# Performance work log

Hardware: AMD Instinct MI355X
Metric: run time of the kernel (lower is better)

Reference implementation:

```python
import jax, jax.numpy as jnp
import numpy as np

H = 1024  # lstm_hidden_dim
E = 1024  # embedding_size
T = 512   # seq_len
B = 128   # batch


def setup_inputs() -> dict:
    key = jax.random.key(0)
    k0, k1, k2, k3 = jax.random.split(key, 4)
    bound = 1.0 / np.sqrt(H)
    embeds = jax.random.normal(k0, (T, B, E), dtype=jnp.float32)
    # Stacked gate weights in order [g, i, f, o]; same math as 8 separate GEMMs.
    W_x = jax.random.uniform(k1, (E, 4 * H), jnp.float32, -bound, bound)
    W_h = jax.random.uniform(k2, (H, 4 * H), jnp.float32, -bound, bound)
    b = jax.random.uniform(k3, (4 * H,), jnp.float32, -bound, bound)
    b = b.at[2 * H:3 * H].add(1.0)  # forget-gate bias +1
    return {"embeds": embeds, "W_x": W_x, "W_h": W_h, "b": b}


def reference(embeds, W_x, W_h, b):
    Tn, Bn, _ = embeds.shape
    # Batch all input projections into one big GEMM (same math as per-step GEMMs).
    xproj = jnp.einsum('tbe,ef->tbf', embeds, W_x) + b  # [T, B, 4H]
    h0 = jnp.zeros((Bn, H), embeds.dtype)
    c0 = jnp.zeros((Bn, H), embeds.dtype)

    def step(carry, xp):
        h, c = carry
        z = xp + h @ W_h  # [B, 4H]
        g = jnp.tanh(z[:, :H])
        i = jax.nn.sigmoid(z[:, H:2 * H])
        f = jax.nn.sigmoid(z[:, 2 * H:3 * H])
        o = jax.nn.sigmoid(z[:, 3 * H:])
        c_new = g * i + c * f
        h_new = jnp.tanh(c_new) * o
        # Original module records h BEFORE the update at step t (h_prev).
        return (h_new, c_new), h

    _, h_total = jax.lax.scan(step, (h0, c0), xproj)
    return h_total  # [T, B, H], h_total[0] is zeros
```

## Files before the change

### kernel.cpp

```cpp
#include <hip/hip_runtime.h>
#include <hip/hip_bf16.h>

typedef __attribute__((ext_vector_type(8)))  short          bf16x8;
typedef __attribute__((ext_vector_type(4)))  float          f32x4;
typedef __attribute__((ext_vector_type(8)))  unsigned short us8;

__device__ __forceinline__ unsigned short f2b(float f) {
  union { __hip_bfloat16 h; unsigned short u; } v;
  v.h = __float2bfloat16(f);
  return v.u;
}
__device__ __forceinline__ float b2f(unsigned short u) {
  union { unsigned u; float f; } v; v.u = ((unsigned)u) << 16; return v.f;
}
__device__ __forceinline__ float sigf(float x) {
  return __builtin_amdgcn_rcpf(1.f + __expf(-x));
}
__device__ __forceinline__ float tanhf_(float x) {
  return 2.f * __builtin_amdgcn_rcpf(1.f + __expf(-2.f * x)) - 1.f;
}


__global__ __launch_bounds__(256) void conv_e(const float* __restrict__ in,
                                              unsigned short* __restrict__ out) {
  const size_t i = ((size_t)blockIdx.x * 256 + threadIdx.x) * 8;
  const float4 v0 = *(const float4*)(in + i);
  const float4 v1 = *(const float4*)(in + i + 4);
  us8 o;
  o[0]=f2b(v0.x); o[1]=f2b(v0.y); o[2]=f2b(v0.z); o[3]=f2b(v0.w);
  o[4]=f2b(v1.x); o[5]=f2b(v1.y); o[6]=f2b(v1.z); o[7]=f2b(v1.w);
  *(us8*)(out + i) = o;
}

__global__ __launch_bounds__(256) void conv_wT(const float* __restrict__ W,
                                               unsigned short* __restrict__ WT) {
  __shared__ float tile[64][65];
  const int bx = blockIdx.x & 63;
  const int by = blockIdx.x >> 6;
  const int tc = threadIdx.x & 63, tr = threadIdx.x >> 6;
  #pragma unroll
  for (int i = 0; i < 16; ++i) {
    const int r = i * 4 + tr;
    tile[r][tc] = W[(size_t)(by * 64 + r) * 4096 + bx * 64 + tc];
  }
  __syncthreads();
  #pragma unroll
  for (int i = 0; i < 16; ++i) {
    const int c = i * 4 + tr;
    WT[(size_t)(bx * 64 + c) * 1024 + by * 64 + tc] = f2b(tile[tc][c]);
  }
}

__global__ __launch_bounds__(256) void conv_whp(const float* __restrict__ Wh,
                                                unsigned short* __restrict__ Wp) {
  const int id = blockIdx.x * 256 + threadIdx.x;
  const int l  = id & 63;
  const int kt = (id >> 6) & 7;
  const int nt = (id >> 9) & 7;
  const int kq = (id >> 12) & 3;
  const int n  = id >> 14;
  const int zi = nt * 16 + (l & 15);
  const int col = (zi >> 5) * 1024 + n * 32 + (zi & 31);
  const int k0 = kq * 256 + kt * 32 + (l >> 4) * 8;
  us8 o;
  #pragma unroll
  for (int j = 0; j < 8; ++j) o[j] = f2b(Wh[(size_t)(k0 + j) * 4096 + col]);
  *(us8*)(Wp + (size_t)id * 8) = o;
}

__global__ __launch_bounds__(256) void gemm_xproj(const unsigned short* __restrict__ A,
                                                  const unsigned short* __restrict__ B,
                                                  unsigned short* __restrict__ C) {
  __shared__ unsigned short Alds[128 * 64];
  __shared__ unsigned short Blds[128 * 64];
  const int tid = threadIdx.x, lane = tid & 63, wv = tid >> 6;
  const int wm = wv >> 1, wn = wv & 1;
  const int bn = blockIdx.x & 31, bm = blockIdx.x >> 5;
  f32x4 acc[4][4] = {};
  const int srow = wv * 8 + (lane >> 3);
  const int sinner = (lane & 7) * 8;
  for (int kt = 0; kt < 16; ++kt) {
    #pragma unroll
    for (int rd = 0; rd < 4; ++rd) {
      const int row = rd * 32 + srow;
      const unsigned short* ga = A + (size_t)(bm * 128 + row) * 1024 + kt * 64 + sinner;
      const unsigned short* gb = B + (size_t)(bn * 128 + row) * 1024 + kt * 64 + sinner;
      __builtin_amdgcn_global_load_lds(
          (const __attribute__((address_space(1))) unsigned short*)ga,
          (__attribute__((address_space(3))) unsigned short*)(Alds + rd * 2048 + wv * 512),
          16, 0, 0);
      __builtin_amdgcn_global_load_lds(
          (const __attribute__((address_space(1))) unsigned short*)gb,
          (__attribute__((address_space(3))) unsigned short*)(Blds + rd * 2048 + wv * 512),
          16, 0, 0);
    }
    __syncthreads();
    #pragma unroll
    for (int ks = 0; ks < 2; ++ks) {
      const int kk = ks * 32 + (lane >> 4) * 8;
      bf16x8 af[4], bfr[4];
      #pragma unroll
      for (int mt = 0; mt < 4; ++mt)
        af[mt] = *(const bf16x8*)(Alds + (wm * 64 + mt * 16 + (lane & 15)) * 64 + kk);
      #pragma unroll
      for (int nt = 0; nt < 4; ++nt)
        bfr[nt] = *(const bf16x8*)(Blds + (wn * 64 + nt * 16 + (lane & 15)) * 64 + kk);
      #pragma unroll
      for (int mt = 0; mt < 4; ++mt)
        #pragma unroll
        for (int nt = 0; nt < 4; ++nt)
          acc[mt][nt] = __builtin_amdgcn_mfma_f32_16x16x32_bf16(af[mt], bfr[nt], acc[mt][nt], 0, 0, 0);
    }
    __syncthreads();
  }
  #pragma unroll
  for (int mt = 0; mt < 4; ++mt) {
    const int row0 = bm * 128 + wm * 64 + mt * 16 + (lane >> 4) * 4;
    #pragma unroll
    for (int nt = 0; nt < 4; ++nt) {
      const int col = bn * 128 + wn * 64 + nt * 16 + (lane & 15);
      #pragma unroll
      for (int r = 0; r < 4; ++r)
        C[(size_t)(row0 + r) * 4096 + col] = f2b(acc[mt][nt][r]);
    }
  }
}

__global__ __launch_bounds__(256, 1) void lstm_recur(
    const unsigned short* __restrict__ xproj,
    const unsigned short* __restrict__ Wp,
    const float* __restrict__ bias,
    unsigned short* __restrict__ hbuf,
    float* __restrict__ out,
    unsigned* __restrict__ flags) {
  __shared__ float zpart[10][16][132];
  const int tid = threadIdx.x;
  const int lane = tid & 63;
  const int kq = tid >> 6;
  const int m = blockIdx.x >> 5;
  const int n = blockIdx.x & 31;

  bf16x8 wf[64];
  {
    const unsigned short* wb = Wp + ((size_t)(n * 4 + kq) * 64) * 512 + lane * 8;
    #pragma unroll
    for (int f = 0; f < 64; ++f) wf[f] = *(const bf16x8*)(wb + f * 512);
  }

  const int r    = tid >> 4;
  const int hg   = tid & 15;
  const int hc0  = n * 32 + hg * 2;
  const int grow = m * 16 + r;

  const float2 bb0 = *(const float2*)(bias +        hc0);
  const float2 bb1 = *(const float2*)(bias + 1024 + hc0);
  const float2 bb2 = *(const float2*)(bias + 2048 + hc0);
  const float2 bb3 = *(const float2*)(bias + 3072 + hc0);

  float cr0 = 0.f, cr1 = 0.f;
  const size_t xbase = (size_t)grow * 4096 + hc0;
  unsigned* bcast = flags + (m * 32 + (lane & 31)) * 32 + n;
  const unsigned* myf = flags + (size_t)(m * 32 + n) * 32 + (lane & 31);

  unsigned xu0, xu1, xu2, xu3;
  {
    const unsigned short* xpp = xproj + xbase;
    asm volatile("global_load_dword %0, %1, off" : "=v"(xu0) : "v"(xpp));
    asm volatile("global_load_dword %0, %1, off" : "=v"(xu1) : "v"(xpp + 1024));
    asm volatile("global_load_dword %0, %1, off" : "=v"(xu2) : "v"(xpp + 2048));
    asm volatile("global_load_dword %0, %1, off" : "=v"(xu3) : "v"(xpp + 3072));
  }

  const size_t aoff = ((size_t)(m * 16 + (lane & 15))) * 1024 + kq * 256 + (lane >> 4) * 8;

  for (int t = 0; t < 511; ++t) {
    const unsigned short* ab = hbuf + (t & 1) * 131072 + aoff;

    bf16x8 av0, av1, av2, av3, av4, av5, av6, av7;
    __builtin_amdgcn_sched_barrier(0);
    asm volatile("global_load_dwordx4 %0, %1, off sc0 sc1"            : "=v"(av0) : "v"(ab));
    asm volatile("global_load_dwordx4 %0, %1, off offset:64 sc0 sc1"  : "=v"(av1) : "v"(ab));
    asm volatile("global_load_dwordx4 %0, %1, off offset:128 sc0 sc1" : "=v"(av2) : "v"(ab));
    asm volatile("global_load_dwordx4 %0, %1, off offset:192 sc0 sc1" : "=v"(av3) : "v"(ab));
    asm volatile("global_load_dwordx4 %0, %1, off offset:256 sc0 sc1" : "=v"(av4) : "v"(ab));
    asm volatile("global_load_dwordx4 %0, %1, off offset:320 sc0 sc1" : "=v"(av5) : "v"(ab));
    asm volatile("global_load_dwordx4 %0, %1, off offset:384 sc0 sc1" : "=v"(av6) : "v"(ab));
    asm volatile("global_load_dwordx4 %0, %1, off offset:448 sc0 sc1" : "=v"(av7) : "v"(ab));
    asm volatile("s_waitcnt vmcnt(0)" ::: "memory");
    __builtin_amdgcn_sched_barrier(0);

    f32x4 ac0 = {0.f,0.f,0.f,0.f}, ac1 = {0.f,0.f,0.f,0.f};
    f32x4 ac2 = {0.f,0.f,0.f,0.f}, ac3 = {0.f,0.f,0.f,0.f};
    f32x4 ac4 = {0.f,0.f,0.f,0.f}, ac5 = {0.f,0.f,0.f,0.f};
    f32x4 ac6 = {0.f,0.f,0.f,0.f}, ac7 = {0.f,0.f,0.f,0.f};
#define MF_STEP(AV, KT) \
    ac0 = __builtin_amdgcn_mfma_f32_16x16x32_bf16(AV, wf[ 0 + KT], ac0, 0, 0, 0); \
    ac1 = __builtin_amdgcn_mfma_f32_16x16x32_bf16(AV, wf[ 8 + KT], ac1, 0, 0, 0); \
    ac2 = __builtin_amdgcn_mfma_f32_16x16x32_bf16(AV, wf[16 + KT], ac2, 0, 0, 0); \
    ac3 = __builtin_amdgcn_mfma_f32_16x16x32_bf16(AV, wf[24 + KT], ac3, 0, 0, 0); \
    ac4 = __builtin_amdgcn_mfma_f32_16x16x32_bf16(AV, wf[32 + KT], ac4, 0, 0, 0); \
    ac5 = __builtin_amdgcn_mfma_f32_16x16x32_bf16(AV, wf[40 + KT], ac5, 0, 0, 0); \
    ac6 = __builtin_amdgcn_mfma_f32_16x16x32_bf16(AV, wf[48 + KT], ac6, 0, 0, 0); \
    ac7 = __builtin_amdgcn_mfma_f32_16x16x32_bf16(AV, wf[56 + KT], ac7, 0, 0, 0);
    MF_STEP(av0, 0) MF_STEP(av1, 1) MF_STEP(av2, 2) MF_STEP(av3, 3)
    MF_STEP(av4, 4) MF_STEP(av5, 5) MF_STEP(av6, 6) MF_STEP(av7, 7)
#undef MF_STEP

    {
      const int crow = (lane >> 4) * 4, ccol = lane & 15;
#define DUMP(NT, AC) \
      zpart[kq][crow + 0][NT * 16 + ccol] = AC[0]; \
      zpart[kq][crow + 1][NT * 16 + ccol] = AC[1]; \
      zpart[kq][crow + 2][NT * 16 + ccol] = AC[2]; \
      zpart[kq][crow + 3][NT * 16 + ccol] = AC[3];
      DUMP(0, ac0) DUMP(1, ac1) DUMP(2, ac2) DUMP(3, ac3)
      DUMP(4, ac4) DUMP(5, ac5) DUMP(6, ac6) DUMP(7, ac7)
#undef DUMP
    }
    __syncthreads();

    float zc[4][2];
    #pragma unroll
    for (int g = 0; g < 4; ++g)
      #pragma unroll
      for (int j = 0; j < 2; ++j) {
        const int col = g * 32 + hg * 2 + j;
        zc[g][j] = (zpart[0][r][col] + zpart[1][r][col])
                 + (zpart[2][r][col] + zpart[3][r][col]);
      }

    float hv0, hv1;
    {
      const float zg = zc[0][0] + b2f((unsigned short)(xu0 & 0xffffu)) + bb0.x;
      const float zi = zc[1][0] + b2f((unsigned short)(xu1 & 0xffffu)) + bb1.x;
      const float zf = zc[2][0] + b2f((unsigned short)(xu2 & 0xffffu)) + bb2.x;
      const float zo = zc[3][0] + b2f((unsigned short)(xu3 & 0xffffu)) + bb3.x;
      cr0 = tanhf_(zg) * sigf(zi) + cr0 * sigf(zf);
      hv0 = tanhf_(cr0) * sigf(zo);
    }
    {
      const float zg = zc[0][1] + b2f((unsigned short)(xu0 >> 16)) + bb0.y;
      const float zi = zc[1][1] + b2f((unsigned short)(xu1 >> 16)) + bb1.y;
      const float zf = zc[2][1] + b2f((unsigned short)(xu2 >> 16)) + bb2.y;
      const float zo = zc[3][1] + b2f((unsigned short)(xu3 >> 16)) + bb3.y;
      cr1 = tanhf_(zg) * sigf(zi) + cr1 * sigf(zf);
      hv1 = tanhf_(cr1) * sigf(zo);
    }

    if (t < 510) {
      const unsigned hp = (unsigned)f2b(hv0) | ((unsigned)f2b(hv1) << 16);
      unsigned short* hd = hbuf + ((t & 1) ^ 1) * 131072 + (size_t)grow * 1024 + hc0;
      asm volatile("global_store_dword %0, %1, off sc0 sc1" :: "v"(hd), "v"(hp) : "memory");
      asm volatile("s_waitcnt vmcnt(0)" ::: "memory");
      __syncthreads();
      if (kq == 0 && lane < 32) {
        const unsigned g1 = (unsigned)(t + 1);
        asm volatile("global_store_dword %0, %1, off sc0 sc1" :: "v"(bcast), "v"(g1) : "memory");
      }
    }

    float2 ho; ho.x = hv0; ho.y = hv1;
    *(float2*)(out + ((size_t)(t + 1) * 128 + grow) * 1024 + hc0) = ho;

    if (t < 510) {
      const unsigned short* xpp = xproj + (size_t)(t + 1) * 524288 + xbase;
      asm volatile("global_load_dword %0, %1, off" : "=v"(xu0) : "v"(xpp));
      asm volatile("global_load_dword %0, %1, off" : "=v"(xu1) : "v"(xpp + 1024));
      asm volatile("global_load_dword %0, %1, off" : "=v"(xu2) : "v"(xpp + 2048));
      asm volatile("global_load_dword %0, %1, off" : "=v"(xu3) : "v"(xpp + 3072));
      unsigned v;
      do {
        asm volatile("global_load_dword %0, %1, off sc0 sc1" : "=v"(v) : "v"(myf));
        asm volatile("s_waitcnt vmcnt(0)" ::: "memory");
      } while (__any((int)v <= t));
    }
  }
}

extern "C" void kernel_launch(void* const* d_in, const int* in_sizes, int n_in,
                              void* d_out, int out_size, void* d_ws, size_t ws_size,
                              hipStream_t stream) {
  (void)in_sizes; (void)n_in; (void)out_size; (void)ws_size;
  const float* embeds = (const float*)d_in[0];
  const float* Wx     = (const float*)d_in[1];
  const float* Wh     = (const float*)d_in[2];
  const float* bias   = (const float*)d_in[3];
  float* out = (float*)d_out;

  char* w = (char*)d_ws;
  unsigned short* eb  = (unsigned short*)(w);
  unsigned short* WxT = (unsigned short*)(w + 134217728);
  unsigned short* Whp = (unsigned short*)(w + 142606336);
  unsigned short* xp  = (unsigned short*)(w + 150994944);
  unsigned short* hb  = (unsigned short*)(w + 687865856);
  unsigned*       fl  = (unsigned*)(w + 688390144);

  hipMemsetAsync(d_out, 0, (size_t)128 * 1024 * sizeof(float), stream);
  hipMemsetAsync(hb, 0, 524288, stream);
  hipMemsetAsync(fl, 0, 32768, stream);

  conv_e   <<<32768, 256, 0, stream>>>(embeds, eb);
  conv_wT  <<<1024,  256, 0, stream>>>(Wx, WxT);
  conv_whp <<<2048,  256, 0, stream>>>(Wh, Whp);
  gemm_xproj<<<16384, 256, 0, stream>>>(eb, WxT, xp);
  lstm_recur<<<256,   256, 0, stream>>>(xp, Whp, bias, hb, out, fl);
}
```

Measured before the change: 2.926 ms.

## Replace flag-based grid sync with tagged h values polled from output

Removes the separate bf16 h buffer and per-block flag array. Each step now writes h straight to the fp32 output, with the low 3 mantissa bits carrying a step-parity tag, and consumers spin on the h data itself until every tag matches. This drops a store-wait-barrier-flag round trip from each step's critical path. It also folds the bias add into the input-projection GEMM epilogue and writes the tagged zeros for step 0 with a small init kernel. In exchange, consumers read fp32 h (twice the bytes) and convert it to bf16 in registers, and the output values lose their low mantissa bits.

```diff
diff --git a/kernel.cpp b/kernel.cpp
--- a/kernel.cpp
+++ b/kernel.cpp
@@ -18,6 +18,11 @@
 }
 __device__ __forceinline__ float tanhf_(float x) {
   return 2.f * __builtin_amdgcn_rcpf(1.f + __expf(-2.f * x)) - 1.f;
+}
+__device__ __forceinline__ unsigned cvtpk(float lo, float hi) {
+  unsigned d;
+  asm("v_cvt_pk_bf16_f32 %0, %1, %2" : "=v"(d) : "v"(lo), "v"(hi));
+  return d;
 }
 
 
@@ -68,8 +73,19 @@
   *(us8*)(Wp + (size_t)id * 8) = o;
 }
 
+__global__ __launch_bounds__(256) void init_out0(unsigned* __restrict__ out) {
+  const unsigned i = (blockIdx.x * 256 + threadIdx.x) * 4;
+  unsigned* p = out + i;
+  const unsigned v = 4u;
+  asm volatile("global_store_dword %0, %1, off sc0 sc1" :: "v"(p),     "v"(v) : "memory");
+  asm volatile("global_store_dword %0, %1, off sc0 sc1" :: "v"(p + 1), "v"(v) : "memory");
+  asm volatile("global_store_dword %0, %1, off sc0 sc1" :: "v"(p + 2), "v"(v) : "memory");
+  asm volatile("global_store_dword %0, %1, off sc0 sc1" :: "v"(p + 3), "v"(v) : "memory");
+}
+
 __global__ __launch_bounds__(256) void gemm_xproj(const unsigned short* __restrict__ A,
                                                   const unsigned short* __restrict__ B,
+                                                  const float* __restrict__ bias,
                                                   unsigned short* __restrict__ C) {
   __shared__ unsigned short Alds[128 * 64];
   __shared__ unsigned short Blds[128 * 64];
@@ -119,9 +135,10 @@
     #pragma unroll
     for (int nt = 0; nt < 4; ++nt) {
       const int col = bn * 128 + wn * 64 + nt * 16 + (lane & 15);
+      const float bv = bias[col];
       #pragma unroll
       for (int r = 0; r < 4; ++r)
-        C[(size_t)(row0 + r) * 4096 + col] = f2b(acc[mt][nt][r]);
+        C[(size_t)(row0 + r) * 4096 + col] = f2b(acc[mt][nt][r] + bv);
     }
   }
 }
@@ -129,10 +146,7 @@
 __global__ __launch_bounds__(256, 1) void lstm_recur(
     const unsigned short* __restrict__ xproj,
     const unsigned short* __restrict__ Wp,
-    const float* __restrict__ bias,
-    unsigned short* __restrict__ hbuf,
-    float* __restrict__ out,
-    unsigned* __restrict__ flags) {
+    float* __restrict__ out) {
   __shared__ float zpart[10][16][132];
   const int tid = threadIdx.x;
   const int lane = tid & 63;
@@ -152,42 +166,58 @@
   const int hc0  = n * 32 + hg * 2;
   const int grow = m * 16 + r;
 
-  const float2 bb0 = *(const float2*)(bias +        hc0);
-  const float2 bb1 = *(const float2*)(bias + 1024 + hc0);
-  const float2 bb2 = *(const float2*)(bias + 2048 + hc0);
-  const float2 bb3 = *(const float2*)(bias + 3072 + hc0);
-
   float cr0 = 0.f, cr1 = 0.f;
   const size_t xbase = (size_t)grow * 4096 + hc0;
-  unsigned* bcast = flags + (m * 32 + (lane & 31)) * 32 + n;
-  const unsigned* myf = flags + (size_t)(m * 32 + n) * 32 + (lane & 31);
-
-  unsigned xu0, xu1, xu2, xu3;
-  {
-    const unsigned short* xpp = xproj + xbase;
-    asm volatile("global_load_dword %0, %1, off" : "=v"(xu0) : "v"(xpp));
-    asm volatile("global_load_dword %0, %1, off" : "=v"(xu1) : "v"(xpp + 1024));
-    asm volatile("global_load_dword %0, %1, off" : "=v"(xu2) : "v"(xpp + 2048));
-    asm volatile("global_load_dword %0, %1, off" : "=v"(xu3) : "v"(xpp + 3072));
-  }
-
-  const size_t aoff = ((size_t)(m * 16 + (lane & 15))) * 1024 + kq * 256 + (lane >> 4) * 8;
+  const size_t abase = ((size_t)(m * 16 + (lane & 15))) * 1024 + kq * 256 + (lane >> 4) * 8;
 
   for (int t = 0; t < 511; ++t) {
-    const unsigned short* ab = hbuf + (t & 1) * 131072 + aoff;
+    unsigned xu0, xu1, xu2, xu3;
+    {
+      const unsigned short* xpp = xproj + (size_t)t * 524288 + xbase;
+      asm volatile("global_load_dword %0, %1, off" : "=v"(xu0) : "v"(xpp));
+      asm volatile("global_load_dword %0, %1, off" : "=v"(xu1) : "v"(xpp + 1024));
+      asm volatile("global_load_dword %0, %1, off" : "=v"(xu2) : "v"(xpp + 2048));
+      asm volatile("global_load_dword %0, %1, off" : "=v"(xu3) : "v"(xpp + 3072));
+    }
+
+    const float* ap = out + (size_t)t * 131072 + abase;
+    const unsigned tagv = 4u | ((unsigned)t & 3u);
+    f32x4 pa0, pa1, pa2, pa3, pa4, pa5, pa6, pa7;
+    f32x4 pb0, pb1, pb2, pb3, pb4, pb5, pb6, pb7;
+
+    while (true) {
+      __builtin_amdgcn_sched_barrier(0);
+#define PLD(PA, PB, OFF) \
+      asm volatile("global_load_dwordx4 %0, %1, off offset:" #OFF " sc0 sc1"      : "=v"(PA) : "v"(ap)); \
+      asm volatile("global_load_dwordx4 %0, %1, off offset:" #OFF "+16 sc0 sc1"   : "=v"(PB) : "v"(ap));
+      PLD(pa0, pb0, 0)   PLD(pa1, pb1, 128) PLD(pa2, pb2, 256) PLD(pa3, pb3, 384)
+      PLD(pa4, pb4, 512) PLD(pa5, pb5, 640) PLD(pa6, pb6, 768) PLD(pa7, pb7, 896)
+#undef PLD
+      asm volatile("s_waitcnt vmcnt(0)" ::: "memory");
+      __builtin_amdgcn_sched_barrier(0);
+      unsigned a0 = 0, a1 = 0, a2 = 0, a3 = 0;
+#define TCHK(PA, PB) \
+      a0 |= __float_as_uint(PA[0]) ^ tagv; a1 |= __float_as_uint(PA[1]) ^ tagv; \
+      a2 |= __float_as_uint(PA[2]) ^ tagv; a3 |= __float_as_uint(PA[3]) ^ tagv; \
+      a0 |= __float_as_uint(PB[0]) ^ tagv; a1 |= __float_as_uint(PB[1]) ^ tagv; \
+      a2 |= __float_as_uint(PB[2]) ^ tagv; a3 |= __float_as_uint(PB[3]) ^ tagv;
+      TCHK(pa0, pb0) TCHK(pa1, pb1) TCHK(pa2, pb2) TCHK(pa3, pb3)
+      TCHK(pa4, pb4) TCHK(pa5, pb5) TCHK(pa6, pb6) TCHK(pa7, pb7)
+#undef TCHK
+      if (__all((int)((((a0 | a1) | (a2 | a3)) & 7u) == 0u))) break;
+      __builtin_amdgcn_s_sleep(1);
+    }
+    __builtin_amdgcn_sched_barrier(0);
 
     bf16x8 av0, av1, av2, av3, av4, av5, av6, av7;
-    __builtin_amdgcn_sched_barrier(0);
-    asm volatile("global_load_dwordx4 %0, %1, off sc0 sc1"            : "=v"(av0) : "v"(ab));
-    asm volatile("global_load_dwordx4 %0, %1, off offset:64 sc0 sc1"  : "=v"(av1) : "v"(ab));
-    asm volatile("global_load_dwordx4 %0, %1, off offset:128 sc0 sc1" : "=v"(av2) : "v"(ab));
-    asm volatile("global_load_dwordx4 %0, %1, off offset:192 sc0 sc1" : "=v"(av3) : "v"(ab));
-    asm volatile("global_load_dwordx4 %0, %1, off offset:256 sc0 sc1" : "=v"(av4) : "v"(ab));
-    asm volatile("global_load_dwordx4 %0, %1, off offset:320 sc0 sc1" : "=v"(av5) : "v"(ab));
-    asm volatile("global_load_dwordx4 %0, %1, off offset:384 sc0 sc1" : "=v"(av6) : "v"(ab));
-    asm volatile("global_load_dwordx4 %0, %1, off offset:448 sc0 sc1" : "=v"(av7) : "v"(ab));
-    asm volatile("s_waitcnt vmcnt(0)" ::: "memory");
-    __builtin_amdgcn_sched_barrier(0);
+#define CVT(AV, PA, PB) { \
+      union { unsigned u[4]; bf16x8 v; } c_; \
+      c_.u[0] = cvtpk(PA[0], PA[1]); c_.u[1] = cvtpk(PA[2], PA[3]); \
+      c_.u[2] = cvtpk(PB[0], PB[1]); c_.u[3] = cvtpk(PB[2], PB[3]); \
+      AV = c_.v; }
+    CVT(av0, pa0, pb0) CVT(av1, pa1, pb1) CVT(av2, pa2, pb2) CVT(av3, pa3, pb3)
+    CVT(av4, pa4, pb4) CVT(av5, pa5, pb5) CVT(av6, pa6, pb6) CVT(av7, pa7, pb7)
+#undef CVT
 
     f32x4 ac0 = {0.f,0.f,0.f,0.f}, ac1 = {0.f,0.f,0.f,0.f};
     f32x4 ac2 = {0.f,0.f,0.f,0.f}, ac3 = {0.f,0.f,0.f,0.f};
@@ -228,51 +258,33 @@
         zc[g][j] = (zpart[0][r][col] + zpart[1][r][col])
                  + (zpart[2][r][col] + zpart[3][r][col]);
       }
+    __syncthreads();
 
     float hv0, hv1;
     {
-      const float zg = zc[0][0] + b2f((unsigned short)(xu0 & 0xffffu)) + bb0.x;
-      const float zi = zc[1][0] + b2f((unsigned short)(xu1 & 0xffffu)) + bb1.x;
-      const float zf = zc[2][0] + b2f((unsigned short)(xu2 & 0xffffu)) + bb2.x;
-      const float zo = zc[3][0] + b2f((unsigned short)(xu3 & 0xffffu)) + bb3.x;
+      const float zg = zc[0][0] + b2f((unsigned short)(xu0 & 0xffffu));
+      const float zi = zc[1][0] + b2f((unsigned short)(xu1 & 0xffffu));
+      const float zf = zc[2][0] + b2f((unsigned short)(xu2 & 0xffffu));
+      const float zo = zc[3][0] + b2f((unsigned short)(xu3 & 0xffffu));
       cr0 = tanhf_(zg) * sigf(zi) + cr0 * sigf(zf);
       hv0 = tanhf_(cr0) * sigf(zo);
     }
     {
-      const float zg = zc[0][1] + b2f((unsigned short)(xu0 >> 16)) + bb0.y;
-      const float zi = zc[1][1] + b2f((unsigned short)(xu1 >> 16)) + bb1.y;
-      const float zf = zc[2][1] + b2f((unsigned short)(xu2 >> 16)) + bb2.y;
-      const float zo = zc[3][1] + b2f((unsigned short)(xu3 >> 16)) + bb3.y;
+      const float zg = zc[0][1] + b2f((unsigned short)(xu0 >> 16));
+      const float zi = zc[1][1] + b2f((unsigned short)(xu1 >> 16));
+      const float zf = zc[2][1] + b2f((unsigned short)(xu2 >> 16));
+      const float zo = zc[3][1] + b2f((unsigned short)(xu3 >> 16));
       cr1 = tanhf_(zg) * sigf(zi) + cr1 * sigf(zf);
       hv1 = tanhf_(cr1) * sigf(zo);
     }
 
-    if (t < 510) {
-      const unsigned hp = (unsigned)f2b(hv0) | ((unsigned)f2b(hv1) << 16);
-      unsigned short* hd = hbuf + ((t & 1) ^ 1) * 131072 + (size_t)grow * 1024 + hc0;
-      asm volatile("global_store_dword %0, %1, off sc0 sc1" :: "v"(hd), "v"(hp) : "memory");
-      asm volatile("s_waitcnt vmcnt(0)" ::: "memory");
-      __syncthreads();
-      if (kq == 0 && lane < 32) {
-        const unsigned g1 = (unsigned)(t + 1);
-        asm volatile("global_store_dword %0, %1, off sc0 sc1" :: "v"(bcast), "v"(g1) : "memory");
-      }
-    }
-
-    float2 ho; ho.x = hv0; ho.y = hv1;
-    *(float2*)(out + ((size_t)(t + 1) * 128 + grow) * 1024 + hc0) = ho;
-
-    if (t < 510) {
-      const unsigned short* xpp = xproj + (size_t)(t + 1) * 524288 + xbase;
-      asm volatile("global_load_dword %0, %1, off" : "=v"(xu0) : "v"(xpp));
-      asm volatile("global_load_dword %0, %1, off" : "=v"(xu1) : "v"(xpp + 1024));
-      asm volatile("global_load_dword %0, %1, off" : "=v"(xu2) : "v"(xpp + 2048));
-      asm volatile("global_load_dword %0, %1, off" : "=v"(xu3) : "v"(xpp + 3072));
-      unsigned v;
-      do {
-        asm volatile("global_load_dword %0, %1, off sc0 sc1" : "=v"(v) : "v"(myf));
-        asm volatile("s_waitcnt vmcnt(0)" ::: "memory");
-      } while (__any((int)v <= t));
+    {
+      const unsigned ptag = 4u | ((unsigned)(t + 1) & 3u);
+      const unsigned u0 = (__float_as_uint(hv0) & ~7u) | ptag;
+      const unsigned u1 = (__float_as_uint(hv1) & ~7u) | ptag;
+      const unsigned long long pk = (unsigned long long)u0 | ((unsigned long long)u1 << 32);
+      float* hd = out + ((size_t)(t + 1) * 131072) + (size_t)grow * 1024 + hc0;
+      asm volatile("global_store_dwordx2 %0, %1, off sc0 sc1" :: "v"(hd), "v"(pk) : "memory");
     }
   }
 }
@@ -292,16 +304,11 @@
   unsigned short* WxT = (unsigned short*)(w + 134217728);
   unsigned short* Whp = (unsigned short*)(w + 142606336);
   unsigned short* xp  = (unsigned short*)(w + 150994944);
-  unsigned short* hb  = (unsigned short*)(w + 687865856);
-  unsigned*       fl  = (unsigned*)(w + 688390144);
-
-  hipMemsetAsync(d_out, 0, (size_t)128 * 1024 * sizeof(float), stream);
-  hipMemsetAsync(hb, 0, 524288, stream);
-  hipMemsetAsync(fl, 0, 32768, stream);
-
-  conv_e   <<<32768, 256, 0, stream>>>(embeds, eb);
-  conv_wT  <<<1024,  256, 0, stream>>>(Wx, WxT);
-  conv_whp <<<2048,  256, 0, stream>>>(Wh, Whp);
-  gemm_xproj<<<16384, 256, 0, stream>>>(eb, WxT, xp);
-  lstm_recur<<<256,   256, 0, stream>>>(xp, Whp, bias, hb, out, fl);
-}
+
+  conv_e    <<<32768, 256, 0, stream>>>(embeds, eb);
+  conv_wT   <<<1024,  256, 0, stream>>>(Wx, WxT);
+  conv_whp  <<<2048,  256, 0, stream>>>(Wh, Whp);
+  init_out0 <<<128,   256, 0, stream>>>((unsigned*)out);
+  gemm_xproj<<<16384, 256, 0, stream>>>(eb, WxT, bias, xp);
+  lstm_recur<<<256,   256, 0, stream>>>(xp, Whp, out);
+}
```

Result: slower. 3.066 ms (+4.8%).

## Fold bias into xproj GEMM, swizzle GEMM blocks, narrow flag polling per wave

Applied to the files above, without the earlier changes.

Adds the gate bias in the xproj GEMM epilogue so the recurrent kernel no longer loads it or adds it every step. This removes four adds per gate pair from the serial recurrence. Remaps GEMM block indices with an XCD-style swizzle, so neighbouring tiles that share operands land on the same chiplet and get better L2 reuse. Changes the flag-polling pointer so each wave watches only its own 8 producer flags instead of all 32. Rounding changes slightly because the bias is now added before the bf16 conversion.

```diff
diff --git a/kernel.cpp b/kernel.cpp
--- a/kernel.cpp
+++ b/kernel.cpp
@@ -70,12 +70,14 @@
 
 __global__ __launch_bounds__(256) void gemm_xproj(const unsigned short* __restrict__ A,
                                                   const unsigned short* __restrict__ B,
+                                                  const float* __restrict__ bias,
                                                   unsigned short* __restrict__ C) {
   __shared__ unsigned short Alds[128 * 64];
   __shared__ unsigned short Blds[128 * 64];
   const int tid = threadIdx.x, lane = tid & 63, wv = tid >> 6;
   const int wm = wv >> 1, wn = wv & 1;
-  const int bn = blockIdx.x & 31, bm = blockIdx.x >> 5;
+  const int sid = (blockIdx.x & 7) * 2048 + (blockIdx.x >> 3);
+  const int bn = sid & 31, bm = sid >> 5;
   f32x4 acc[4][4] = {};
   const int srow = wv * 8 + (lane >> 3);
   const int sinner = (lane & 7) * 8;
@@ -119,9 +121,10 @@
     #pragma unroll
     for (int nt = 0; nt < 4; ++nt) {
       const int col = bn * 128 + wn * 64 + nt * 16 + (lane & 15);
+      const float bv = bias[col];
       #pragma unroll
       for (int r = 0; r < 4; ++r)
-        C[(size_t)(row0 + r) * 4096 + col] = f2b(acc[mt][nt][r]);
+        C[(size_t)(row0 + r) * 4096 + col] = f2b(acc[mt][nt][r] + bv);
     }
   }
 }
@@ -129,7 +132,6 @@
 __global__ __launch_bounds__(256, 1) void lstm_recur(
     const unsigned short* __restrict__ xproj,
     const unsigned short* __restrict__ Wp,
-    const float* __restrict__ bias,
     unsigned short* __restrict__ hbuf,
     float* __restrict__ out,
     unsigned* __restrict__ flags) {
@@ -152,15 +154,10 @@
   const int hc0  = n * 32 + hg * 2;
   const int grow = m * 16 + r;
 
-  const float2 bb0 = *(const float2*)(bias +        hc0);
-  const float2 bb1 = *(const float2*)(bias + 1024 + hc0);
-  const float2 bb2 = *(const float2*)(bias + 2048 + hc0);
-  const float2 bb3 = *(const float2*)(bias + 3072 + hc0);
-
   float cr0 = 0.f, cr1 = 0.f;
   const size_t xbase = (size_t)grow * 4096 + hc0;
   unsigned* bcast = flags + (m * 32 + (lane & 31)) * 32 + n;
-  const unsigned* myf = flags + (size_t)(m * 32 + n) * 32 + (lane & 31);
+  const unsigned* myf = flags + (size_t)(m * 32 + n) * 32 + kq * 8 + (lane & 7);
 
   unsigned xu0, xu1, xu2, xu3;
   {
@@ -231,18 +228,18 @@
 
     float hv0, hv1;
     {
-      const float zg = zc[0][0] + b2f((unsigned short)(xu0 & 0xffffu)) + bb0.x;
-      const float zi = zc[1][0] + b2f((unsigned short)(xu1 & 0xffffu)) + bb1.x;
-      const float zf = zc[2][0] + b2f((unsigned short)(xu2 & 0xffffu)) + bb2.x;
-      const float zo = zc[3][0] + b2f((unsigned short)(xu3 & 0xffffu)) + bb3.x;
+      const float zg = zc[0][0] + b2f((unsigned short)(xu0 & 0xffffu));
+      const float zi = zc[1][0] + b2f((unsigned short)(xu1 & 0xffffu));
+      const float zf = zc[2][0] + b2f((unsigned short)(xu2 & 0xffffu));
+      const float zo = zc[3][0] + b2f((unsigned short)(xu3 & 0xffffu));
       cr0 = tanhf_(zg) * sigf(zi) + cr0 * sigf(zf);
       hv0 = tanhf_(cr0) * sigf(zo);
     }
     {
-      const float zg = zc[0][1] + b2f((unsigned short)(xu0 >> 16)) + bb0.y;
-      const float zi = zc[1][1] + b2f((unsigned short)(xu1 >> 16)) + bb1.y;
-      const float zf = zc[2][1] + b2f((unsigned short)(xu2 >> 16)) + bb2.y;
-      const float zo = zc[3][1] + b2f((unsigned short)(xu3 >> 16)) + bb3.y;
+      const float zg = zc[0][1] + b2f((unsigned short)(xu0 >> 16));
+      const float zi = zc[1][1] + b2f((unsigned short)(xu1 >> 16));
+      const float zf = zc[2][1] + b2f((unsigned short)(xu2 >> 16));
+      const float zo = zc[3][1] + b2f((unsigned short)(xu3 >> 16));
       cr1 = tanhf_(zg) * sigf(zi) + cr1 * sigf(zf);
       hv1 = tanhf_(cr1) * sigf(zo);
     }
@@ -299,9 +296,9 @@
   hipMemsetAsync(hb, 0, 524288, stream);
   hipMemsetAsync(fl, 0, 32768, stream);
 
-  conv_e   <<<32768, 256, 0, stream>>>(embeds, eb);
-  conv_wT  <<<1024,  256, 0, stream>>>(Wx, WxT);
-  conv_whp <<<2048,  256, 0, stream>>>(Wh, Whp);
-  gemm_xproj<<<16384, 256, 0, stream>>>(eb, WxT, xp);
-  lstm_recur<<<256,   256, 0, stream>>>(xp, Whp, bias, hb, out, fl);
-}
+  conv_e    <<<32768, 256, 0, stream>>>(embeds, eb);
+  conv_wT   <<<1024,  256, 0, stream>>>(Wx, WxT);
+  conv_whp  <<<2048,  256, 0, stream>>>(Wh, Whp);
+  gemm_xproj<<<16384, 256, 0, stream>>>(eb, WxT, bias, xp);
+  lstm_recur<<<256,   256, 0, stream>>>(xp, Whp, hb, out, fl);
+}
```

Measured after the change: 2.919 ms. Within noise of the previous version (-0.2%).
